# Performance work log

Hardware: AMD Instinct MI355X
Metric: run time of the kernel (lower is better)

The kernel has to match this reference:

```python
import jax, jax.numpy as jnp
import numpy as np

N_AGENTS = 32
STATE_DIM = 512
LATENT = 16
H = 64  # attention_hidden_dim
N1 = N_AGENTS
N2 = N_AGENTS * (N_AGENTS - 1) // 2
NF = N1 + N2
B = 32768
# pairwise indices, same order as itertools.combinations(range(n), 2)
_PI, _PJ = np.triu_indices(N_AGENTS, k=1)
PI = jnp.asarray(_PI)
PJ = jnp.asarray(_PJ)


def setup_inputs() -> dict:
    key = jax.random.key(0)
    ks = jax.random.split(key, 24)
    s = 0.1  # small init scale (xavier gain 0.5)
    inp = {
        "agent_q_values": jax.random.normal(ks[0], (B, N_AGENTS), jnp.float32),
        "state": jax.random.normal(ks[1], (B, STATE_DIM), jnp.float32),
        "agent_semantics": jax.random.normal(ks[2], (B, N_AGENTS, LATENT), jnp.float32),
        # order-1 shape functions, stacked over N1 functions, weights in [in,out] layout
        "w1_1": jax.random.normal(ks[3], (N1, 1, 8), jnp.float32) * s,
        "b1_1": jnp.zeros((N1, 8), jnp.float32),
        "w2_1": jax.random.normal(ks[4], (N1, 8, 4), jnp.float32) * s,
        "b2_1": jnp.zeros((N1, 4), jnp.float32),
        "w3_1": jax.random.normal(ks[5], (N1, 4, 1), jnp.float32) * s,
        "b3_1": jnp.zeros((N1, 1), jnp.float32),
        # order-2 shape functions, stacked over N2 pairs
        "w1_2": jax.random.normal(ks[6], (N2, 2, 8), jnp.float32) * s,
        "b1_2": jnp.zeros((N2, 8), jnp.float32),
        "w2_2": jax.random.normal(ks[7], (N2, 8, 4), jnp.float32) * s,
        "b2_2": jnp.zeros((N2, 4), jnp.float32),
        "w3_2": jax.random.normal(ks[8], (N2, 4, 1), jnp.float32) * s,
        "b3_2": jnp.zeros((N2, 1), jnp.float32),
        # state encoder
        "ws_w": jax.random.normal(ks[9], (STATE_DIM, H), jnp.float32) * (1.0 / np.sqrt(STATE_DIM)),
        "ws_b": jnp.zeros((H,), jnp.float32),
        # semantic encoder
        "wz_w": jax.random.normal(ks[10], (LATENT * N_AGENTS, H), jnp.float32) * (1.0 / np.sqrt(LATENT * N_AGENTS)),
        "wz_b": jnp.zeros((H,), jnp.float32),
        # attention net
        "wa1_w": jax.random.normal(ks[11], (2 * H, H), jnp.float32) * (1.0 / np.sqrt(2 * H)),
        "wa1_b": jnp.zeros((H,), jnp.float32),
        "wa2_w": jax.random.normal(ks[12], (H, NF), jnp.float32) * (1.0 / np.sqrt(H)),
        "wa2_b": jnp.zeros((NF,), jnp.float32),
        # bias net
        "wb1_w": jax.random.normal(ks[13], (STATE_DIM, H), jnp.float32) * (1.0 / np.sqrt(STATE_DIM)),
        "wb1_b": jnp.zeros((H,), jnp.float32),
        "wb2_w": jax.random.normal(ks[14], (H, 1), jnp.float32) * (1.0 / np.sqrt(H)),
        "wb2_b": jnp.zeros((1,), jnp.float32),
    }
    return inp


def _shape_fns(x, w1, b1, w2, b2, w3, b3):
    # x: [B, N, D_in]; weights stacked over N functions; abs() on weights (monotonicity)
    h = jax.nn.elu(jnp.einsum("bnd,ndh->bnh", x, jnp.abs(w1)) + b1)   # [B,N,8]
    h = jax.nn.elu(jnp.einsum("bnh,nhk->bnk", h, jnp.abs(w2)) + b2)   # [B,N,4]
    f = jnp.einsum("bnk,nk->bn", h, jnp.abs(w3)[:, :, 0]) + b3[:, 0]  # [B,N]
    return f


def reference(agent_q_values, state, agent_semantics,
              w1_1, b1_1, w2_1, b2_1, w3_1, b3_1,
              w1_2, b1_2, w2_2, b2_2, w3_2, b3_2,
              ws_w, ws_b, wz_w, wz_b,
              wa1_w, wa1_b, wa2_w, wa2_b,
              wb1_w, wb1_b, wb2_w, wb2_b):
    q = agent_q_values  # [B, n_agents]
    # order-1 shape functions: input is scalar Q_i
    f1 = _shape_fns(q[:, :, None], w1_1, b1_1, w2_1, b2_1, w3_1, b3_1)   # [B, N1]
    # order-2 shape functions: input is [Q_i, Q_j] per pair
    q_pairs = jnp.stack([q[:, PI], q[:, PJ]], axis=-1)                    # [B, N2, 2]
    f2 = _shape_fns(q_pairs, w1_2, b1_2, w2_2, b2_2, w3_2, b3_2)          # [B, N2]
    shape_outputs = jnp.concatenate([f1, f2], axis=-1)                    # [B, NF]

    state_enc = jax.nn.relu(state @ ws_w + ws_b)                          # [B, H]
    sem_flat = agent_semantics.reshape(agent_semantics.shape[0], -1)      # [B, n*latent]
    sem_enc = jax.nn.relu(sem_flat @ wz_w + wz_b)                         # [B, H]
    combined = jnp.concatenate([state_enc, sem_enc], axis=-1)             # [B, 2H]
    logits = jax.nn.relu(combined @ wa1_w + wa1_b) @ wa2_w + wa2_b        # [B, NF]
    attention_weights = jax.nn.softmax(logits, axis=-1)

    weighted_sum = jnp.sum(attention_weights * shape_outputs, axis=-1, keepdims=True)
    bias = jax.nn.relu(state @ wb1_w + wb1_b) @ wb2_w + wb2_b             # [B, 1]
    q_total = weighted_sum + bias
    return (q_total, attention_weights, shape_outputs)
```

## Files before the change

kernel.cpp:

```cpp
#include <hip/hip_runtime.h>
#include <cstdint>
#include <cstddef>

#define NAG 32
#define N1C 32
#define N2C 496
#define NF 528
#define HD 64
#define SD 512

typedef __attribute__((ext_vector_type(8))) short bf16x8;
typedef __attribute__((ext_vector_type(4))) float f32x4;
#define MFMA16(a, b, c) __builtin_amdgcn_mfma_f32_16x16x32_bf16(a, b, c, 0, 0, 0)

__device__ __forceinline__ unsigned short f2bf(float f) {
    unsigned int u = __float_as_uint(f);
    u += 0x7fffu + ((u >> 16) & 1u);
    return (unsigned short)(u >> 16);
}
__device__ __forceinline__ unsigned int pack2(float a, float b) {
    return (unsigned int)f2bf(a) | ((unsigned int)f2bf(b) << 16);
}
__device__ __forceinline__ float elu_f(float x) {
    return x > 0.f ? x : (__expf(x) - 1.f);
}

#define OFF_WST   0
#define OFF_WB1T  32768
#define OFF_WZT   65536
#define OFF_WA1T  98304
#define OFF_WA2T  106496
#define PREP_TOT  140288

__global__ __launch_bounds__(256) void prep_kernel(
    const float* __restrict__ ws_w, const float* __restrict__ wb1_w,
    const float* __restrict__ wz_w, const float* __restrict__ wa1_w,
    const float* __restrict__ wa2_w, unsigned short* __restrict__ ws)
{
    int i = blockIdx.x * 256 + threadIdx.x;
    if (i >= PREP_TOT) return;
    float v;
    if (i < OFF_WB1T) {
        int j = i - OFF_WST; int n = j >> 9, k = j & 511;
        v = ws_w[k * 64 + n];
    } else if (i < OFF_WZT) {
        int j = i - OFF_WB1T; int n = j >> 9, k = j & 511;
        v = wb1_w[k * 64 + n];
    } else if (i < OFF_WA1T) {
        int j = i - OFF_WZT; int n = j >> 9, k = j & 511;
        v = wz_w[k * 64 + n];
    } else if (i < OFF_WA2T) {
        int j = i - OFF_WA1T; int n = j >> 7, k = j & 127;
        v = wa1_w[k * 64 + n];
    } else {
        int j = i - OFF_WA2T; int n = j >> 6, k = j & 63;
        v = wa2_w[k * NF + n];
    }
    ws[i] = f2bf(v);
}

#define SROWS 64
__global__ __launch_bounds__(576) void shape_kernel(
    const float* __restrict__ q,
    const float* __restrict__ w1_1, const float* __restrict__ b1_1,
    const float* __restrict__ w2_1, const float* __restrict__ b2_1,
    const float* __restrict__ w3_1, const float* __restrict__ b3_1,
    const float* __restrict__ w1_2, const float* __restrict__ b1_2,
    const float* __restrict__ w2_2, const float* __restrict__ b2_2,
    const float* __restrict__ w3_2, const float* __restrict__ b3_2,
    float* __restrict__ shape_out, int B)
{
    __shared__ float qs[SROWS][NAG];

    int tid = threadIdx.x;
    int f = tid;
    bool valid = f < NF;
    int fe = valid ? f : (NF - 1);

    float w1a[8], w1b[8], b1v[8], w2v[32], b2v[4], w3v[4], b3v;
    int pi, pj;
    if (fe < N1C) {
        int n = fe;
        pi = n; pj = n;
        #pragma unroll
        for (int k = 0; k < 8; k++) { w1a[k] = fabsf(w1_1[n*8+k]); w1b[k] = 0.f; b1v[k] = b1_1[n*8+k]; }
        #pragma unroll
        for (int t = 0; t < 32; t++) w2v[t] = fabsf(w2_1[n*32+t]);
        #pragma unroll
        for (int j = 0; j < 4; j++) { b2v[j] = b2_1[n*4+j]; w3v[j] = fabsf(w3_1[n*4+j]); }
        b3v = b3_1[n];
    } else {
        int n = fe - N1C;
        int p = n, i = 0, c = NAG - 1;
        while (p >= c) { p -= c; c--; i++; }
        pi = i; pj = i + 1 + p;
        #pragma unroll
        for (int k = 0; k < 8; k++) { w1a[k] = fabsf(w1_2[n*16+k]); w1b[k] = fabsf(w1_2[n*16+8+k]); b1v[k] = b1_2[n*8+k]; }
        #pragma unroll
        for (int t = 0; t < 32; t++) w2v[t] = fabsf(w2_2[n*32+t]);
        #pragma unroll
        for (int j = 0; j < 4; j++) { b2v[j] = b2_2[n*4+j]; w3v[j] = fabsf(w3_2[n*4+j]); }
        b3v = b3_2[n];
    }

    int row0 = blockIdx.x * SROWS;
    if (tid < 512) {
        float4 v = *(const float4*)&q[(size_t)row0 * NAG + tid * 4];
        *(float4*)&((float*)qs)[tid * 4] = v;
    }
    __syncthreads();

    #pragma unroll 4
    for (int rr = 0; rr < SROWS; rr++) {
        float qi = qs[rr][pi];
        float qj = qs[rr][pj];
        float h1[8];
        #pragma unroll
        for (int k = 0; k < 8; k++) h1[k] = elu_f(w1a[k]*qi + w1b[k]*qj + b1v[k]);
        float h2[4];
        #pragma unroll
        for (int j = 0; j < 4; j++) {
            float a = b2v[j];
            #pragma unroll
            for (int k = 0; k < 8; k++) a += h1[k] * w2v[k*4 + j];
            h2[j] = elu_f(a);
        }
        float fv = b3v;
        #pragma unroll
        for (int j = 0; j < 4; j++) fv += h2[j] * w3v[j];
        if (valid) shape_out[(size_t)(row0 + rr) * NF + f] = fv;
    }
}

#define RB 64
__global__ __launch_bounds__(256, 2) void enc_mfma(
    const float* __restrict__ state,
    const float* __restrict__ sem,
    const unsigned short* __restrict__ wsbuf,
    const float* __restrict__ ws_b, const float* __restrict__ wz_b,
    const float* __restrict__ wa1_b, const float* __restrict__ wa2_b,
    const float* __restrict__ wb1_b, const float* __restrict__ wb2_w,
    const float* __restrict__ wb2_b,
    const float* __restrict__ shape_out,
    float* __restrict__ q_total,
    float* __restrict__ attn_out)
{
    __shared__ unsigned short sComb[RB][136];
    __shared__ unsigned short sH[RB][72];

    const unsigned short* wsT  = wsbuf + OFF_WST;
    const unsigned short* wb1T = wsbuf + OFF_WB1T;
    const unsigned short* wzT  = wsbuf + OFF_WZT;
    const unsigned short* wa1T = wsbuf + OFF_WA1T;
    const unsigned short* wa2T = wsbuf + OFF_WA2T;

    int tid  = threadIdx.x;
    int lane = tid & 63;
    int w    = tid >> 6;
    int col  = lane & 15;
    int quad = lane >> 4;
    int r0   = blockIdx.x * RB;
    int rowt = w * 16;

    const float* __restrict__ srowS = state + (size_t)(r0 + rowt + col) * SD + quad * 8;
    const float* __restrict__ srowZ = sem   + (size_t)(r0 + rowt + col) * SD + quad * 8;
    const unsigned short* __restrict__ bS0 = wsT  + col * SD + quad * 8;
    const unsigned short* __restrict__ bB0 = wb1T + col * SD + quad * 8;
    const unsigned short* __restrict__ bZ0 = wzT  + col * SD + quad * 8;

    f32x4 accS[4], accB[4], accZ[4];
    #pragma unroll
    for (int ct = 0; ct < 4; ct++) {
        accS[ct] = (f32x4){0.f,0.f,0.f,0.f};
        accB[ct] = (f32x4){0.f,0.f,0.f,0.f};
        accZ[ct] = (f32x4){0.f,0.f,0.f,0.f};
    }

    #pragma unroll 2
    for (int ks = 0; ks < 16; ks++) {
        float4 s0 = *(const float4*)(srowS + ks * 32);
        float4 s1 = *(const float4*)(srowS + ks * 32 + 4);
        float4 z0 = *(const float4*)(srowZ + ks * 32);
        float4 z1 = *(const float4*)(srowZ + ks * 32 + 4);
        bf16x8 as, az;
        {
            unsigned int* p = (unsigned int*)&as;
            p[0] = pack2(s0.x, s0.y); p[1] = pack2(s0.z, s0.w);
            p[2] = pack2(s1.x, s1.y); p[3] = pack2(s1.z, s1.w);
            unsigned int* pz = (unsigned int*)&az;
            pz[0] = pack2(z0.x, z0.y); pz[1] = pack2(z0.z, z0.w);
            pz[2] = pack2(z1.x, z1.y); pz[3] = pack2(z1.z, z1.w);
        }
        int wof = ks * 32;
        #pragma unroll
        for (int ct = 0; ct < 4; ct++) {
            bf16x8 bS = *(const bf16x8*)(bS0 + ct * 16 * SD + wof);
            bf16x8 bB = *(const bf16x8*)(bB0 + ct * 16 * SD + wof);
            bf16x8 bZ = *(const bf16x8*)(bZ0 + ct * 16 * SD + wof);
            accS[ct] = MFMA16(as, bS, accS[ct]);
            accB[ct] = MFMA16(as, bB, accB[ct]);
            accZ[ct] = MFMA16(az, bZ, accZ[ct]);
        }
    }

    #pragma unroll
    for (int ct = 0; ct < 4; ct++) {
        float bs = ws_b[ct * 16 + col];
        float bz = wz_b[ct * 16 + col];
        #pragma unroll
        for (int reg = 0; reg < 4; reg++) {
            int rr = rowt + quad * 4 + reg;
            sComb[rr][ct * 16 + col]      = f2bf(fmaxf(accS[ct][reg] + bs, 0.f));
            sComb[rr][64 + ct * 16 + col] = f2bf(fmaxf(accZ[ct][reg] + bz, 0.f));
        }
    }
    __syncthreads();

    float qbv[4];
    #pragma unroll
    for (int reg = 0; reg < 4; reg++) {
        float p = 0.f;
        #pragma unroll
        for (int ct = 0; ct < 4; ct++)
            p += fmaxf(accB[ct][reg] + wb1_b[ct * 16 + col], 0.f) * wb2_w[ct * 16 + col];
        #pragma unroll
        for (int m = 1; m < 16; m <<= 1) p += __shfl_xor(p, m, 64);
        qbv[reg] = p;
    }

    f32x4 accH[4];
    #pragma unroll
    for (int ct = 0; ct < 4; ct++) accH[ct] = (f32x4){0.f,0.f,0.f,0.f};
    #pragma unroll
    for (int ks = 0; ks < 4; ks++) {
        bf16x8 a = *(const bf16x8*)&sComb[rowt + col][ks * 32 + quad * 8];
        #pragma unroll
        for (int ct = 0; ct < 4; ct++) {
            bf16x8 b = *(const bf16x8*)&wa1T[(ct * 16 + col) * 128 + ks * 32 + quad * 8];
            accH[ct] = MFMA16(a, b, accH[ct]);
        }
    }
    #pragma unroll
    for (int ct = 0; ct < 4; ct++) {
        float bh = wa1_b[ct * 16 + col];
        #pragma unroll
        for (int reg = 0; reg < 4; reg++)
            sH[rowt + quad * 4 + reg][ct * 16 + col] = f2bf(fmaxf(accH[ct][reg] + bh, 0.f));
    }
    __syncthreads();

    bf16x8 ha0 = *(const bf16x8*)&sH[rowt + col][quad * 8];
    bf16x8 ha1 = *(const bf16x8*)&sH[rowt + col][32 + quad * 8];

    float sAcc[4] = {0.f,0.f,0.f,0.f};
    float wAcc[4] = {0.f,0.f,0.f,0.f};
    for (int nt = 0; nt < 33; nt++) {
        f32x4 acc = (f32x4){0.f,0.f,0.f,0.f};
        const unsigned short* wp = &wa2T[(nt * 16 + col) * 64 + quad * 8];
        acc = MFMA16(ha0, *(const bf16x8*)wp, acc);
        acc = MFMA16(ha1, *(const bf16x8*)(wp + 32), acc);
        float lb = wa2_b[nt * 16 + col];
        #pragma unroll
        for (int reg = 0; reg < 4; reg++) {
            float e = __expf(acc[reg] + lb);
            sAcc[reg] += e;
            wAcc[reg] += e * shape_out[(size_t)(r0 + rowt + quad * 4 + reg) * NF + nt * 16 + col];
        }
    }
    float inv[4];
    #pragma unroll
    for (int reg = 0; reg < 4; reg++) {
        float s = sAcc[reg], ww = wAcc[reg];
        #pragma unroll
        for (int m = 1; m < 16; m <<= 1) { s += __shfl_xor(s, m, 64); ww += __shfl_xor(ww, m, 64); }
        inv[reg] = 1.f / s;
        if (col == 0)
            q_total[r0 + rowt + quad * 4 + reg] = ww * inv[reg] + qbv[reg] + wb2_b[0];
    }

    for (int nt = 0; nt < 33; nt++) {
        f32x4 acc = (f32x4){0.f,0.f,0.f,0.f};
        const unsigned short* wp = &wa2T[(nt * 16 + col) * 64 + quad * 8];
        acc = MFMA16(ha0, *(const bf16x8*)wp, acc);
        acc = MFMA16(ha1, *(const bf16x8*)(wp + 32), acc);
        float lb = wa2_b[nt * 16 + col];
        #pragma unroll
        for (int reg = 0; reg < 4; reg++) {
            float e = __expf(acc[reg] + lb);
            attn_out[(size_t)(r0 + rowt + quad * 4 + reg) * NF + nt * 16 + col] = e * inv[reg];
        }
    }
}

extern "C" void kernel_launch(void* const* d_in, const int* in_sizes, int n_in,
                              void* d_out, int out_size, void* d_ws, size_t ws_size,
                              hipStream_t stream) {
    const float* q     = (const float*)d_in[0];
    const float* state = (const float*)d_in[1];
    const float* sem   = (const float*)d_in[2];
    const float* w1_1  = (const float*)d_in[3];
    const float* b1_1  = (const float*)d_in[4];
    const float* w2_1  = (const float*)d_in[5];
    const float* b2_1  = (const float*)d_in[6];
    const float* w3_1  = (const float*)d_in[7];
    const float* b3_1  = (const float*)d_in[8];
    const float* w1_2  = (const float*)d_in[9];
    const float* b1_2  = (const float*)d_in[10];
    const float* w2_2  = (const float*)d_in[11];
    const float* b2_2  = (const float*)d_in[12];
    const float* w3_2  = (const float*)d_in[13];
    const float* b3_2  = (const float*)d_in[14];
    const float* ws_w  = (const float*)d_in[15];
    const float* ws_b  = (const float*)d_in[16];
    const float* wz_w  = (const float*)d_in[17];
    const float* wz_b  = (const float*)d_in[18];
    const float* wa1_w = (const float*)d_in[19];
    const float* wa1_b = (const float*)d_in[20];
    const float* wa2_w = (const float*)d_in[21];
    const float* wa2_b = (const float*)d_in[22];
    const float* wb1_w = (const float*)d_in[23];
    const float* wb1_b = (const float*)d_in[24];
    const float* wb2_w = (const float*)d_in[25];
    const float* wb2_b = (const float*)d_in[26];

    int B = in_sizes[0] / NAG;

    float* out_q    = (float*)d_out;
    float* out_attn = out_q + B;
    float* out_shp  = out_attn + (size_t)B * NF;

    unsigned short* wsbuf = (unsigned short*)d_ws;

    prep_kernel<<<(PREP_TOT + 255) / 256, 256, 0, stream>>>(
        ws_w, wb1_w, wz_w, wa1_w, wa2_w, wsbuf);

    shape_kernel<<<B / SROWS, 576, 0, stream>>>(q,
        w1_1, b1_1, w2_1, b2_1, w3_1, b3_1,
        w1_2, b1_2, w2_2, b2_2, w3_2, b3_2,
        out_shp, B);

    enc_mfma<<<B / RB, 256, 0, stream>>>(state, sem, wsbuf,
        ws_b, wz_b, wa1_b, wa2_b, wb1_b, wb2_w, wb2_b,
        out_shp, out_q, out_attn);
}
```

Baseline: 419.1 us.

## Split encoder work across warps by output tile instead of by row block

The encoder kernel now processes 16 rows per block instead of 64. Its four warps divide the 12 output column tiles of the state, bias and semantic GEMMs among themselves, and also split the 33 attention-logit tiles round-robin. Partial softmax sums and bias contributions are combined through shared memory. This gives 4x more blocks with fewer registers each (launch bounds raised to 6 blocks per SM), aiming for better occupancy and latency hiding. In exchange, each block rereads all weight tiles for only 16 rows, adds extra syncs and shared-memory reductions, and loads the state/sem rows redundantly across warps.

```diff
diff --git a/kernel.cpp b/kernel.cpp
--- a/kernel.cpp
+++ b/kernel.cpp
@@ -132,8 +132,97 @@
     }
 }
 
-#define RB 64
-__global__ __launch_bounds__(256, 2) void enc_mfma(
+#define RB 16
+
+template<int T>
+__device__ __forceinline__ void tile_epi(const f32x4& acc,
+    const float* __restrict__ ws_b, const float* __restrict__ wz_b,
+    const float* __restrict__ wb1_b, const float* __restrict__ wb2_w,
+    int col, int quad, unsigned short (*sComb)[136], float* pbias)
+{
+    constexpr int G = T >> 2, C = T & 3;
+    if constexpr (G == 0) {
+        float b = ws_b[C*16 + col];
+        #pragma unroll
+        for (int r = 0; r < 4; r++)
+            sComb[quad*4 + r][C*16 + col] = f2bf(fmaxf(acc[r] + b, 0.f));
+    } else if constexpr (G == 2) {
+        float b = wz_b[C*16 + col];
+        #pragma unroll
+        for (int r = 0; r < 4; r++)
+            sComb[quad*4 + r][64 + C*16 + col] = f2bf(fmaxf(acc[r] + b, 0.f));
+    } else {
+        float b = wb1_b[C*16 + col], w2 = wb2_w[C*16 + col];
+        #pragma unroll
+        for (int r = 0; r < 4; r++)
+            pbias[r] += fmaxf(acc[r] + b, 0.f) * w2;
+    }
+}
+
+template<int W>
+__device__ __forceinline__ void phase1(
+    const float* __restrict__ srowS, const float* __restrict__ srowZ,
+    const unsigned short* __restrict__ wsbuf,
+    const float* __restrict__ ws_b, const float* __restrict__ wz_b,
+    const float* __restrict__ wb1_b, const float* __restrict__ wb2_w,
+    int col, int quad,
+    unsigned short (*sComb)[136], float (*sBias)[16])
+{
+    constexpr int T0 = W*3, T1 = W*3 + 1, T2 = W*3 + 2;
+    constexpr bool needS = (T0 < 8);
+    constexpr bool needZ = (T2 >= 8);
+
+    constexpr int G0 = T0 >> 2, C0 = T0 & 3;
+    constexpr int G1 = T1 >> 2, C1 = T1 & 3;
+    constexpr int G2 = T2 >> 2, C2 = T2 & 3;
+    const unsigned short* bp0 = wsbuf + (G0==0?OFF_WST:G0==1?OFF_WB1T:OFF_WZT) + (C0*16 + col)*SD + quad*8;
+    const unsigned short* bp1 = wsbuf + (G1==0?OFF_WST:G1==1?OFF_WB1T:OFF_WZT) + (C1*16 + col)*SD + quad*8;
+    const unsigned short* bp2 = wsbuf + (G2==0?OFF_WST:G2==1?OFF_WB1T:OFF_WZT) + (C2*16 + col)*SD + quad*8;
+
+    f32x4 a0 = {0.f,0.f,0.f,0.f};
+    f32x4 a1 = {0.f,0.f,0.f,0.f};
+    f32x4 a2 = {0.f,0.f,0.f,0.f};
+
+    #pragma unroll 2
+    for (int ks = 0; ks < 16; ks++) {
+        bf16x8 as = {}, az = {};
+        if constexpr (needS) {
+            float4 s0 = *(const float4*)(srowS + ks*32);
+            float4 s1 = *(const float4*)(srowS + ks*32 + 4);
+            unsigned int* p = (unsigned int*)&as;
+            p[0] = pack2(s0.x, s0.y); p[1] = pack2(s0.z, s0.w);
+            p[2] = pack2(s1.x, s1.y); p[3] = pack2(s1.z, s1.w);
+        }
+        if constexpr (needZ) {
+            float4 z0 = *(const float4*)(srowZ + ks*32);
+            float4 z1 = *(const float4*)(srowZ + ks*32 + 4);
+            unsigned int* p = (unsigned int*)&az;
+            p[0] = pack2(z0.x, z0.y); p[1] = pack2(z0.z, z0.w);
+            p[2] = pack2(z1.x, z1.y); p[3] = pack2(z1.z, z1.w);
+        }
+        int wof = ks * 32;
+        a0 = MFMA16((T0 >= 8) ? az : as, *(const bf16x8*)(bp0 + wof), a0);
+        a1 = MFMA16((T1 >= 8) ? az : as, *(const bf16x8*)(bp1 + wof), a1);
+        a2 = MFMA16((T2 >= 8) ? az : as, *(const bf16x8*)(bp2 + wof), a2);
+    }
+
+    float pbias[4] = {0.f, 0.f, 0.f, 0.f};
+    tile_epi<T0>(a0, ws_b, wz_b, wb1_b, wb2_w, col, quad, sComb, pbias);
+    tile_epi<T1>(a1, ws_b, wz_b, wb1_b, wb2_w, col, quad, sComb, pbias);
+    tile_epi<T2>(a2, ws_b, wz_b, wb1_b, wb2_w, col, quad, sComb, pbias);
+
+    if constexpr (W == 1 || W == 2) {
+        #pragma unroll
+        for (int r = 0; r < 4; r++) {
+            float p = pbias[r];
+            #pragma unroll
+            for (int m = 1; m < 16; m <<= 1) p += __shfl_xor(p, m, 64);
+            if (col == 0) sBias[W - 1][quad*4 + r] = p;
+        }
+    }
+}
+
+__global__ __launch_bounds__(256, 6) void enc_mfma(
     const float* __restrict__ state,
     const float* __restrict__ sem,
     const unsigned short* __restrict__ wsbuf,
@@ -147,10 +236,10 @@
 {
     __shared__ unsigned short sComb[RB][136];
     __shared__ unsigned short sH[RB][72];
-
-    const unsigned short* wsT  = wsbuf + OFF_WST;
-    const unsigned short* wb1T = wsbuf + OFF_WB1T;
-    const unsigned short* wzT  = wsbuf + OFF_WZT;
+    __shared__ float sBias[2][RB];
+    __shared__ float sRedS[4][RB];
+    __shared__ float sRedW[4][RB];
+
     const unsigned short* wa1T = wsbuf + OFF_WA1T;
     const unsigned short* wa2T = wsbuf + OFF_WA2T;
 
@@ -160,134 +249,82 @@
     int col  = lane & 15;
     int quad = lane >> 4;
     int r0   = blockIdx.x * RB;
-    int rowt = w * 16;
-
-    const float* __restrict__ srowS = state + (size_t)(r0 + rowt + col) * SD + quad * 8;
-    const float* __restrict__ srowZ = sem   + (size_t)(r0 + rowt + col) * SD + quad * 8;
-    const unsigned short* __restrict__ bS0 = wsT  + col * SD + quad * 8;
-    const unsigned short* __restrict__ bB0 = wb1T + col * SD + quad * 8;
-    const unsigned short* __restrict__ bZ0 = wzT  + col * SD + quad * 8;
-
-    f32x4 accS[4], accB[4], accZ[4];
-    #pragma unroll
-    for (int ct = 0; ct < 4; ct++) {
-        accS[ct] = (f32x4){0.f,0.f,0.f,0.f};
-        accB[ct] = (f32x4){0.f,0.f,0.f,0.f};
-        accZ[ct] = (f32x4){0.f,0.f,0.f,0.f};
-    }
-
-    #pragma unroll 2
-    for (int ks = 0; ks < 16; ks++) {
-        float4 s0 = *(const float4*)(srowS + ks * 32);
-        float4 s1 = *(const float4*)(srowS + ks * 32 + 4);
-        float4 z0 = *(const float4*)(srowZ + ks * 32);
-        float4 z1 = *(const float4*)(srowZ + ks * 32 + 4);
-        bf16x8 as, az;
-        {
-            unsigned int* p = (unsigned int*)&as;
-            p[0] = pack2(s0.x, s0.y); p[1] = pack2(s0.z, s0.w);
-            p[2] = pack2(s1.x, s1.y); p[3] = pack2(s1.z, s1.w);
-            unsigned int* pz = (unsigned int*)&az;
-            pz[0] = pack2(z0.x, z0.y); pz[1] = pack2(z0.z, z0.w);
-            pz[2] = pack2(z1.x, z1.y); pz[3] = pack2(z1.z, z1.w);
-        }
-        int wof = ks * 32;
-        #pragma unroll
-        for (int ct = 0; ct < 4; ct++) {
-            bf16x8 bS = *(const bf16x8*)(bS0 + ct * 16 * SD + wof);
-            bf16x8 bB = *(const bf16x8*)(bB0 + ct * 16 * SD + wof);
-            bf16x8 bZ = *(const bf16x8*)(bZ0 + ct * 16 * SD + wof);
-            accS[ct] = MFMA16(as, bS, accS[ct]);
-            accB[ct] = MFMA16(as, bB, accB[ct]);
-            accZ[ct] = MFMA16(az, bZ, accZ[ct]);
-        }
-    }
-
-    #pragma unroll
-    for (int ct = 0; ct < 4; ct++) {
-        float bs = ws_b[ct * 16 + col];
-        float bz = wz_b[ct * 16 + col];
-        #pragma unroll
-        for (int reg = 0; reg < 4; reg++) {
-            int rr = rowt + quad * 4 + reg;
-            sComb[rr][ct * 16 + col]      = f2bf(fmaxf(accS[ct][reg] + bs, 0.f));
-            sComb[rr][64 + ct * 16 + col] = f2bf(fmaxf(accZ[ct][reg] + bz, 0.f));
-        }
+
+    const float* srowS = state + (size_t)(r0 + col) * SD + quad * 8;
+    const float* srowZ = sem   + (size_t)(r0 + col) * SD + quad * 8;
+
+    switch (w) {
+        case 0:  phase1<0>(srowS, srowZ, wsbuf, ws_b, wz_b, wb1_b, wb2_w, col, quad, sComb, sBias); break;
+        case 1:  phase1<1>(srowS, srowZ, wsbuf, ws_b, wz_b, wb1_b, wb2_w, col, quad, sComb, sBias); break;
+        case 2:  phase1<2>(srowS, srowZ, wsbuf, ws_b, wz_b, wb1_b, wb2_w, col, quad, sComb, sBias); break;
+        default: phase1<3>(srowS, srowZ, wsbuf, ws_b, wz_b, wb1_b, wb2_w, col, quad, sComb, sBias); break;
     }
     __syncthreads();
 
-    float qbv[4];
-    #pragma unroll
-    for (int reg = 0; reg < 4; reg++) {
-        float p = 0.f;
-        #pragma unroll
-        for (int ct = 0; ct < 4; ct++)
-            p += fmaxf(accB[ct][reg] + wb1_b[ct * 16 + col], 0.f) * wb2_w[ct * 16 + col];
-        #pragma unroll
-        for (int m = 1; m < 16; m <<= 1) p += __shfl_xor(p, m, 64);
-        qbv[reg] = p;
-    }
-
-    f32x4 accH[4];
-    #pragma unroll
-    for (int ct = 0; ct < 4; ct++) accH[ct] = (f32x4){0.f,0.f,0.f,0.f};
+    f32x4 accH = {0.f,0.f,0.f,0.f};
     #pragma unroll
     for (int ks = 0; ks < 4; ks++) {
-        bf16x8 a = *(const bf16x8*)&sComb[rowt + col][ks * 32 + quad * 8];
-        #pragma unroll
-        for (int ct = 0; ct < 4; ct++) {
-            bf16x8 b = *(const bf16x8*)&wa1T[(ct * 16 + col) * 128 + ks * 32 + quad * 8];
-            accH[ct] = MFMA16(a, b, accH[ct]);
-        }
-    }
-    #pragma unroll
-    for (int ct = 0; ct < 4; ct++) {
-        float bh = wa1_b[ct * 16 + col];
-        #pragma unroll
-        for (int reg = 0; reg < 4; reg++)
-            sH[rowt + quad * 4 + reg][ct * 16 + col] = f2bf(fmaxf(accH[ct][reg] + bh, 0.f));
+        bf16x8 a = *(const bf16x8*)&sComb[col][ks*32 + quad*8];
+        bf16x8 b = *(const bf16x8*)&wa1T[(w*16 + col)*128 + ks*32 + quad*8];
+        accH = MFMA16(a, b, accH);
+    }
+    {
+        float bh = wa1_b[w*16 + col];
+        #pragma unroll
+        for (int r = 0; r < 4; r++)
+            sH[quad*4 + r][w*16 + col] = f2bf(fmaxf(accH[r] + bh, 0.f));
     }
     __syncthreads();
 
-    bf16x8 ha0 = *(const bf16x8*)&sH[rowt + col][quad * 8];
-    bf16x8 ha1 = *(const bf16x8*)&sH[rowt + col][32 + quad * 8];
+    bf16x8 ha0 = *(const bf16x8*)&sH[col][quad*8];
+    bf16x8 ha1 = *(const bf16x8*)&sH[col][32 + quad*8];
 
     float sAcc[4] = {0.f,0.f,0.f,0.f};
     float wAcc[4] = {0.f,0.f,0.f,0.f};
-    for (int nt = 0; nt < 33; nt++) {
-        f32x4 acc = (f32x4){0.f,0.f,0.f,0.f};
-        const unsigned short* wp = &wa2T[(nt * 16 + col) * 64 + quad * 8];
+    for (int nt = w; nt < 33; nt += 4) {
+        f32x4 acc = {0.f,0.f,0.f,0.f};
+        const unsigned short* wp = &wa2T[(nt*16 + col)*64 + quad*8];
         acc = MFMA16(ha0, *(const bf16x8*)wp, acc);
         acc = MFMA16(ha1, *(const bf16x8*)(wp + 32), acc);
-        float lb = wa2_b[nt * 16 + col];
-        #pragma unroll
-        for (int reg = 0; reg < 4; reg++) {
-            float e = __expf(acc[reg] + lb);
-            sAcc[reg] += e;
-            wAcc[reg] += e * shape_out[(size_t)(r0 + rowt + quad * 4 + reg) * NF + nt * 16 + col];
-        }
-    }
+        float lb = wa2_b[nt*16 + col];
+        #pragma unroll
+        for (int r = 0; r < 4; r++) {
+            float e = __expf(acc[r] + lb);
+            sAcc[r] += e;
+            wAcc[r] += e * shape_out[(size_t)(r0 + quad*4 + r) * NF + nt*16 + col];
+        }
+    }
+    #pragma unroll
+    for (int r = 0; r < 4; r++) {
+        float s = sAcc[r], ww = wAcc[r];
+        #pragma unroll
+        for (int m = 1; m < 16; m <<= 1) { s += __shfl_xor(s, m, 64); ww += __shfl_xor(ww, m, 64); }
+        if (col == 0) { sRedS[w][quad*4 + r] = s; sRedW[w][quad*4 + r] = ww; }
+    }
+    __syncthreads();
+
     float inv[4];
     #pragma unroll
-    for (int reg = 0; reg < 4; reg++) {
-        float s = sAcc[reg], ww = wAcc[reg];
-        #pragma unroll
-        for (int m = 1; m < 16; m <<= 1) { s += __shfl_xor(s, m, 64); ww += __shfl_xor(ww, m, 64); }
-        inv[reg] = 1.f / s;
-        if (col == 0)
-            q_total[r0 + rowt + quad * 4 + reg] = ww * inv[reg] + qbv[reg] + wb2_b[0];
-    }
-
-    for (int nt = 0; nt < 33; nt++) {
-        f32x4 acc = (f32x4){0.f,0.f,0.f,0.f};
-        const unsigned short* wp = &wa2T[(nt * 16 + col) * 64 + quad * 8];
+    for (int r = 0; r < 4; r++) {
+        int row = quad*4 + r;
+        float st = sRedS[0][row] + sRedS[1][row] + sRedS[2][row] + sRedS[3][row];
+        inv[r] = 1.f / st;
+        if (w == 0 && col == 0) {
+            float wt = sRedW[0][row] + sRedW[1][row] + sRedW[2][row] + sRedW[3][row];
+            q_total[r0 + row] = wt * inv[r] + sBias[0][row] + sBias[1][row] + wb2_b[0];
+        }
+    }
+
+    for (int nt = w; nt < 33; nt += 4) {
+        f32x4 acc = {0.f,0.f,0.f,0.f};
+        const unsigned short* wp = &wa2T[(nt*16 + col)*64 + quad*8];
         acc = MFMA16(ha0, *(const bf16x8*)wp, acc);
         acc = MFMA16(ha1, *(const bf16x8*)(wp + 32), acc);
-        float lb = wa2_b[nt * 16 + col];
-        #pragma unroll
-        for (int reg = 0; reg < 4; reg++) {
-            float e = __expf(acc[reg] + lb);
-            attn_out[(size_t)(r0 + rowt + quad * 4 + reg) * NF + nt * 16 + col] = e * inv[reg];
+        float lb = wa2_b[nt*16 + col];
+        #pragma unroll
+        for (int r = 0; r < 4; r++) {
+            float e = __expf(acc[r] + lb);
+            attn_out[(size_t)(r0 + quad*4 + r) * NF + nt*16 + col] = e * inv[r];
         }
     }
 }
```

Result: slower. 451.2 us (+7.6%).
